# Performance work log

Measured on AMD Instinct MI355X. Metric: run time of the kernel, lower is better.

Reference implementation:

```python
import jax, jax.numpy as jnp
import numpy as np

E = 512      # room_emb_size
H = 8        # nhead
HD = E // H  # head dim
F = 32       # dim_feedforward (hardcoded in source)
L = 3        # num_layers
V = 32000    # voc_size
B = 128      # batch
T = 16       # max_sent_len == max_length
SOS = 1      # sos_idx
EPS = 1e-5   # torch LayerNorm eps


def setup_inputs() -> dict:
    key = jax.random.key(0)
    ks = jax.random.split(key, 10)
    s = 0.02
    def rn(k, shape):
        return jax.random.normal(k, shape, jnp.float32) * s
    return {
        "cur_room_emb": jax.random.normal(ks[0], (B, E), jnp.float32),
        "emb": rn(ks[1], (V, E)),
        "sa_in_w": rn(ks[2], (L, 3 * E, E)), "sa_in_b": jnp.zeros((L, 3 * E), jnp.float32),
        "sa_out_w": rn(ks[3], (L, E, E)), "sa_out_b": jnp.zeros((L, E), jnp.float32),
        "ca_in_w": rn(ks[4], (L, 3 * E, E)), "ca_in_b": jnp.zeros((L, 3 * E), jnp.float32),
        "ca_out_w": rn(ks[5], (L, E, E)), "ca_out_b": jnp.zeros((L, E), jnp.float32),
        "ff1_w": rn(ks[6], (L, F, E)), "ff1_b": jnp.zeros((L, F), jnp.float32),
        "ff2_w": rn(ks[7], (L, E, F)), "ff2_b": jnp.zeros((L, E), jnp.float32),
        "ln_g": jnp.ones((L, 3, E), jnp.float32), "ln_b": jnp.zeros((L, 3, E), jnp.float32),
        "out_w": rn(ks[8], (V, E)), "out_b": jnp.zeros((V,), jnp.float32),
        "max_length": T,
    }


def _ln(x, g, b):
    m = jnp.mean(x, axis=-1, keepdims=True)
    v = jnp.mean((x - m) ** 2, axis=-1, keepdims=True)
    return (x - m) / jnp.sqrt(v + EPS) * g + b


def _mha(qx, kvx, in_w, in_b, out_w, out_b):
    # qx: [Sq,B,E], kvx: [Sk,B,E]  (torch seq-first layout)
    wq, wk, wv = in_w[:E], in_w[E:2 * E], in_w[2 * E:]
    bq, bk, bv = in_b[:E], in_b[E:2 * E], in_b[2 * E:]
    q = (qx @ wq.T + bq).reshape(qx.shape[0], -1, H, HD)
    k = (kvx @ wk.T + bk).reshape(kvx.shape[0], -1, H, HD)
    v = (kvx @ wv.T + bv).reshape(kvx.shape[0], -1, H, HD)
    att = jax.nn.softmax(jnp.einsum('qbhd,kbhd->bhqk', q, k) / np.sqrt(HD).astype(np.float32), axis=-1)
    o = jnp.einsum('bhqk,kbhd->qbhd', att, v).reshape(qx.shape[0], -1, E)
    return o @ out_w.T + out_b


def _pos_enc(n):
    pos = np.arange(n)[:, None].astype(np.float32)
    div = np.exp(np.arange(0, E, 2).astype(np.float32) * (-np.log(10000.0) / E))
    pe = np.zeros((n, E), np.float32)
    pe[:, 0::2] = np.sin(pos * div)
    pe[:, 1::2] = np.cos(pos * div)
    return jnp.asarray(pe)


def reference(cur_room_emb, emb, sa_in_w, sa_in_b, sa_out_w, sa_out_b,
              ca_in_w, ca_in_b, ca_out_w, ca_out_b,
              ff1_w, ff1_b, ff2_w, ff2_b, ln_g, ln_b, out_w, out_b, max_length):
    pe = _pos_enc(max_length)
    bsz = cur_room_emb.shape[0]
    hx = cur_room_emb[None]  # memory [1,B,E]
    # initial <sos> embedding (no positional encoding, as in the source)
    tok_before = jnp.broadcast_to(emb[SOS][None, None, :], (1, bsz, E))
    tokens, probs_all = [], []
    for i in range(max_length):
        x = tok_before  # rerun full decoder over growing history (faithful, no KV cache)
        for l in range(L):
            x = _ln(x + _mha(x, x, sa_in_w[l], sa_in_b[l], sa_out_w[l], sa_out_b[l]), ln_g[l, 0], ln_b[l, 0])
            x = _ln(x + _mha(x, hx, ca_in_w[l], ca_in_b[l], ca_out_w[l], ca_out_b[l]), ln_g[l, 1], ln_b[l, 1])
            ff = jax.nn.relu(x @ ff1_w[l].T + ff1_b[l]) @ ff2_w[l].T + ff2_b[l]
            x = _ln(x + ff, ln_g[l, 2], ln_b[l, 2])
        probs = jax.nn.softmax(x[-1] @ out_w.T + out_b, axis=1)  # emb2idx: Linear + Softmax(dim=1)
        tok = jnp.argmax(probs, axis=1)  # greedy token choice (deterministic)
        tokens.append(tok)
        probs_all.append(probs)
        new = (emb[tok] + pe[i])[None]  # [1,B,E]: embed + positional(i)
        tok_before = jnp.concatenate([tok_before, new], axis=0)
    spoken_token = jnp.stack(tokens, axis=0).T  # [B, max_length]
    return spoken_token, jnp.stack(probs_all, axis=0)  # probs: [T,B,V]
```

## Files before the change

### kernel.cpp

```cpp
#include <hip/hip_runtime.h>
#include <hip/hip_bf16.h>
#include <math.h>

#define E   512
#define E3  1536
#define NH  8
#define FF  32
#define NL  3
#define NV  32000
#define NB  128
#define NT  16
#define RESCUE_DELTA 0.08f

typedef __attribute__((ext_vector_type(8))) short bf16x8;
typedef __attribute__((ext_vector_type(4))) float f32x4;

__global__ void setup_kernel(float* __restrict__ pe, float* __restrict__ tb,
                             const float* __restrict__ emb) {
    const int bi = blockIdx.x;
    if (bi < 16) {
        for (int e = threadIdx.x; e < E; e += blockDim.x) {
            int k = e >> 1;
            double dv = exp((double)(2 * k) * (-log(10000.0) / (double)E));
            double arg = (double)bi * dv;
            pe[bi * E + e] = (e & 1) ? (float)cos(arg) : (float)sin(arg);
        }
    } else {
        const int b = bi - 16;
        for (int e = threadIdx.x; e < E; e += blockDim.x)
            tb[(size_t)b * E + e] = emb[(size_t)1 * E + e];
    }
}

__global__ __launch_bounds__(256) void cvt_bf16_kernel(
    const float* __restrict__ src, unsigned short* __restrict__ dst)
{
    const int i = (blockIdx.x * 256 + threadIdx.x) * 4;
    const float4 v = *(const float4*)&src[i];
    __hip_bfloat16 h0 = __float2bfloat16(v.x);
    __hip_bfloat16 h1 = __float2bfloat16(v.y);
    __hip_bfloat16 h2 = __float2bfloat16(v.z);
    __hip_bfloat16 h3 = __float2bfloat16(v.w);
    dst[i + 0] = *(unsigned short*)&h0;
    dst[i + 1] = *(unsigned short*)&h1;
    dst[i + 2] = *(unsigned short*)&h2;
    dst[i + 3] = *(unsigned short*)&h3;
}

__global__ __launch_bounds__(256) void ca_setup_kernel(
    const float* __restrict__ cur_room,
    const float* __restrict__ ca_in_w, const float* __restrict__ ca_in_b,
    const float* __restrict__ ca_out_w, const float* __restrict__ ca_out_b,
    float* __restrict__ ca_const)
{
    const int b = blockIdx.x, l = blockIdx.y, t = threadIdx.x;
    __shared__ float xl[E];
    __shared__ float hv[E];
    for (int e = t; e < E; e += 256) xl[e] = cur_room[(size_t)b * E + e];
    __syncthreads();
    const float* wv = ca_in_w + ((size_t)l * E3 + 2 * E) * E;
    const float* bv = ca_in_b + (size_t)l * E3 + 2 * E;
    for (int c = t; c < E; c += 256) {
        float s = bv[c];
        const float* wr = wv + (size_t)c * E;
        for (int k = 0; k < E; ++k) s += xl[k] * wr[k];
        hv[c] = s;
    }
    __syncthreads();
    const float* wo = ca_out_w + (size_t)l * E * E;
    for (int c = t; c < E; c += 256) {
        float s = ca_out_b[(size_t)l * E + c];
        const float* wr = wo + (size_t)c * E;
        for (int k = 0; k < E; ++k) s += hv[k] * wr[k];
        ca_const[((size_t)l * NB + b) * E + c] = s;
    }
}

template<bool ADD_BIAS>
__global__ __launch_bounds__(256) void gemm_v3_kernel(
    const float* __restrict__ A, const float* __restrict__ W,
    const float* __restrict__ bias, float* __restrict__ C,
    int N, int K, int KC, size_t CS, int skipm)
{
    const int m0 = blockIdx.y * 64;
    const int n0 = blockIdx.x * 128;
    if (n0 < E && m0 < skipm) return;
    __shared__ float As[16][68];
    __shared__ float Bs[16][132];
    const int tid = threadIdx.x;
    const int kc0 = blockIdx.z * KC;
    const int tx = tid & 15;
    const int ty = tid >> 4;
    const int sr = tid >> 2;
    const int sc = (tid & 3) * 4;

    const float* Ap  = A + (size_t)(m0 + sr) * K + kc0 + sc;
    const float* Wp0 = W + (size_t)(n0 + sr) * K + kc0 + sc;
    const float* Wp1 = W + (size_t)(n0 + 64 + sr) * K + kc0 + sc;

    float4 pa  = *(const float4*)Ap;
    float4 pb0 = *(const float4*)Wp0;
    float4 pb1 = *(const float4*)Wp1;

    float acc[4][8] = {};
    const int nkt = KC >> 4;
    for (int kt = 0; kt < nkt; ++kt) {
        __syncthreads();
        As[sc + 0][sr] = pa.x;  As[sc + 1][sr] = pa.y;
        As[sc + 2][sr] = pa.z;  As[sc + 3][sr] = pa.w;
        Bs[sc + 0][sr] = pb0.x; Bs[sc + 1][sr] = pb0.y;
        Bs[sc + 2][sr] = pb0.z; Bs[sc + 3][sr] = pb0.w;
        Bs[sc + 0][64 + sr] = pb1.x; Bs[sc + 1][64 + sr] = pb1.y;
        Bs[sc + 2][64 + sr] = pb1.z; Bs[sc + 3][64 + sr] = pb1.w;
        __syncthreads();
        if (kt + 1 < nkt) {
            const int off = 16 * (kt + 1);
            pa  = *(const float4*)(Ap + off);
            pb0 = *(const float4*)(Wp0 + off);
            pb1 = *(const float4*)(Wp1 + off);
        }
#pragma unroll
        for (int k = 0; k < 16; ++k) {
            float a[4], b[8];
            *(float4*)&a[0] = *(const float4*)&As[k][ty * 4];
            *(float4*)&b[0] = *(const float4*)&Bs[k][tx * 4];
            *(float4*)&b[4] = *(const float4*)&Bs[k][64 + tx * 4];
#pragma unroll
            for (int i = 0; i < 4; ++i)
#pragma unroll
                for (int j = 0; j < 8; ++j)
                    acc[i][j] += a[i] * b[j];
        }
    }
    float* Co = C + (size_t)blockIdx.z * CS;
#pragma unroll
    for (int i = 0; i < 4; ++i) {
        const int m = m0 + ty * 4 + i;
#pragma unroll
        for (int cj = 0; cj < 2; ++cj) {
            const int n = n0 + cj * 64 + tx * 4;
            float4 o;
            o.x = acc[i][cj * 4 + 0];
            o.y = acc[i][cj * 4 + 1];
            o.z = acc[i][cj * 4 + 2];
            o.w = acc[i][cj * 4 + 3];
            if (ADD_BIAS) {
                const float4 bv = *(const float4*)&bias[n];
                o.x += bv.x; o.y += bv.y; o.z += bv.z; o.w += bv.w;
            }
            *(float4*)&Co[(size_t)m * N + n] = o;
        }
    }
}

__global__ __launch_bounds__(256) void vgemm_bf16_kernel(
    const unsigned short* __restrict__ Abf,
    const unsigned short* __restrict__ Wbf,
    const float* __restrict__ bias, float* __restrict__ Cout)
{
    const int wid = threadIdx.x >> 6, lane = threadIdx.x & 63;
    const int n0 = (blockIdx.x * 4 + wid) * 32;
    const int r = lane & 15;
    const int ko = (lane >> 4) * 8;
    f32x4 acc[2][8];
#pragma unroll
    for (int nt = 0; nt < 2; ++nt)
#pragma unroll
        for (int m = 0; m < 8; ++m)
            acc[nt][m] = (f32x4){0.f, 0.f, 0.f, 0.f};

    const unsigned short* a0 = Abf + (size_t)r * E + ko;
    const unsigned short* w0 = Wbf + (size_t)(n0 + r) * E + ko;
    const unsigned short* w1 = Wbf + (size_t)(n0 + 16 + r) * E + ko;
    for (int k0 = 0; k0 < E; k0 += 32) {
        const bf16x8 b0 = *(const bf16x8*)(w0 + k0);
        const bf16x8 b1 = *(const bf16x8*)(w1 + k0);
#pragma unroll
        for (int m = 0; m < 8; ++m) {
            const bf16x8 af = *(const bf16x8*)(a0 + (size_t)m * 16 * E + k0);
            acc[0][m] = __builtin_amdgcn_mfma_f32_16x16x32_bf16(af, b0, acc[0][m], 0, 0, 0);
            acc[1][m] = __builtin_amdgcn_mfma_f32_16x16x32_bf16(af, b1, acc[1][m], 0, 0, 0);
        }
    }
    const int crow = (lane >> 4) * 4;
#pragma unroll
    for (int nt = 0; nt < 2; ++nt) {
        const int col = n0 + nt * 16 + r;
        const float bv = bias[col];
#pragma unroll
        for (int m = 0; m < 8; ++m)
#pragma unroll
            for (int rr = 0; rr < 4; ++rr)
                Cout[(size_t)(m * 16 + crow + rr) * NV + col] = acc[nt][m][rr] + bv;
    }
}

template<bool WB>
__global__ __launch_bounds__(128) void attn_kernel(
    const float* __restrict__ qkv, size_t QS, int pcount,
    const float* __restrict__ cache, float* __restrict__ wbdst,
    const float* __restrict__ bias,
    float* __restrict__ o, int S, int qstart)
{
    const int b = blockIdx.x >> 3;
    const int h = blockIdx.x & 7;
    __shared__ float Ks[16][64];
    __shared__ float Vs[16][64];
    const int tid = threadIdx.x;
    if (WB) {
        for (int e = tid; e < 192; e += 128) {
            const int part = e >> 6, d = e & 63;
            const int go = part * E + h * 64 + d;
            float v = 0.f;
#pragma unroll
            for (int p = 0; p < 8; ++p) v += qkv[(size_t)p * QS + (size_t)b * E3 + go];
            wbdst[(size_t)b * E3 + go] = v;
            if (part == 1) Ks[S - 1][d] = v + bias[go];
            else if (part == 2) Vs[S - 1][d] = v + bias[go];
        }
        for (int idx = tid; idx < (S - 1) * 64; idx += 128) {
            const int s = idx >> 6, d = idx & 63;
            const size_t base = ((size_t)(s * NB + b)) * E3 + h * 64 + d;
            Ks[s][d] = cache[base + E] + bias[E + h * 64 + d];
            Vs[s][d] = cache[base + 2 * E] + bias[2 * E + h * 64 + d];
        }
    } else {
        for (int idx = tid; idx < S * 64; idx += 128) {
            const int s = idx >> 6, d = idx & 63;
            const size_t base = ((size_t)(s * NB + b)) * E3 + h * 64 + d;
            float kk = bias[E + h * 64 + d];
            float vv = bias[2 * E + h * 64 + d];
            for (int p = 0; p < pcount; ++p) {
                kk += qkv[(size_t)p * QS + base + E];
                vv += qkv[(size_t)p * QS + base + 2 * E];
            }
            Ks[s][d] = kk;
            Vs[s][d] = vv;
        }
    }
    __syncthreads();
    const int wid = tid >> 6, lane = tid & 63;
    const float bq = bias[h * 64 + lane];
    for (int qi = qstart + wid; qi < S; qi += 2) {
        const size_t qbase = ((size_t)(qi * NB + b)) * E3 + h * 64 + lane;
        float qd = bq;
        if (WB) qd += cache[qbase];
        else for (int p = 0; p < pcount; ++p) qd += qkv[(size_t)p * QS + qbase];
        float sc[16];
#pragma unroll
        for (int ki = 0; ki < 16; ++ki) {
            float p = 0.f;
            if (ki < S) {
                p = qd * Ks[ki][lane];
#pragma unroll
                for (int off = 32; off; off >>= 1) p += __shfl_xor(p, off);
                p *= 0.125f;
            }
            sc[ki] = p;
        }
        float m = -1e30f;
#pragma unroll
        for (int ki = 0; ki < 16; ++ki) if (ki < S) m = fmaxf(m, sc[ki]);
        float sum = 0.f;
#pragma unroll
        for (int ki = 0; ki < 16; ++ki) if (ki < S) { sc[ki] = expf(sc[ki] - m); sum += sc[ki]; }
        float inv = 1.0f / sum;
        float acc = 0.f;
#pragma unroll
        for (int ki = 0; ki < 16; ++ki) if (ki < S) acc += sc[ki] * Vs[ki][lane];
        o[((size_t)(qi * NB + b)) * E + h * 64 + lane] = acc * inv;
    }
}

__global__ __launch_bounds__(256) void epilogue_kernel(
    const float* __restrict__ xin,
    const float* __restrict__ yp, size_t YS, int pcount,
    const float* __restrict__ ob,
    const float* __restrict__ ca,
    const float* __restrict__ g0, const float* __restrict__ b0,
    const float* __restrict__ g1, const float* __restrict__ b1,
    const float* __restrict__ w1, const float* __restrict__ b1f,
    const float* __restrict__ w2, const float* __restrict__ b2f,
    const float* __restrict__ g2, const float* __restrict__ bb2,
    float* __restrict__ xout, unsigned short* __restrict__ xbf, int rows)
{
    const int wid = threadIdx.x >> 6, lane = threadIdx.x & 63;
    const int row = blockIdx.x * 4 + wid;
    if (row >= rows) return;
    const float* xr = xin + (size_t)row * E;
    const float* cr = ca + (size_t)(row & (NB - 1)) * E;
    float v[8];
    float s = 0.f;
#pragma unroll
    for (int j = 0; j < 8; ++j) {
        int e = j * 64 + lane;
        float y = xr[e] + ob[e];
        for (int p = 0; p < pcount; ++p) y += yp[(size_t)p * YS + (size_t)row * E + e];
        v[j] = y; s += y;
    }
#pragma unroll
    for (int off = 32; off; off >>= 1) s += __shfl_xor(s, off);
    float mean = s * (1.0f / E);
    float vs = 0.f;
#pragma unroll
    for (int j = 0; j < 8; ++j) { float d = v[j] - mean; vs += d * d; }
#pragma unroll
    for (int off = 32; off; off >>= 1) vs += __shfl_xor(vs, off);
    float rstd = rsqrtf(vs * (1.0f / E) + 1e-5f);
#pragma unroll
    for (int j = 0; j < 8; ++j) {
        int e = j * 64 + lane;
        v[j] = (v[j] - mean) * rstd * g0[e] + b0[e] + cr[e];
    }
    s = 0.f;
#pragma unroll
    for (int j = 0; j < 8; ++j) s += v[j];
#pragma unroll
    for (int off = 32; off; off >>= 1) s += __shfl_xor(s, off);
    mean = s * (1.0f / E);
    vs = 0.f;
#pragma unroll
    for (int j = 0; j < 8; ++j) { float d = v[j] - mean; vs += d * d; }
#pragma unroll
    for (int off = 32; off; off >>= 1) vs += __shfl_xor(vs, off);
    rstd = rsqrtf(vs * (1.0f / E) + 1e-5f);
#pragma unroll
    for (int j = 0; j < 8; ++j) {
        int e = j * 64 + lane;
        v[j] = (v[j] - mean) * rstd * g1[e] + b1[e];
    }
    float h[FF];
#pragma unroll
    for (int f = 0; f < FF; ++f) {
        float p = 0.f;
#pragma unroll
        for (int j = 0; j < 8; ++j) p += v[j] * w1[(size_t)f * E + j * 64 + lane];
#pragma unroll
        for (int off = 32; off; off >>= 1) p += __shfl_xor(p, off);
        h[f] = fmaxf(p + b1f[f], 0.f);
    }
    float o[8];
#pragma unroll
    for (int j = 0; j < 8; ++j) {
        int e = j * 64 + lane;
        float acc = b2f[e];
#pragma unroll
        for (int f4 = 0; f4 < FF / 4; ++f4) {
            float4 w4 = *(const float4*)&w2[(size_t)e * FF + f4 * 4];
            acc += h[f4 * 4 + 0] * w4.x + h[f4 * 4 + 1] * w4.y +
                   h[f4 * 4 + 2] * w4.z + h[f4 * 4 + 3] * w4.w;
        }
        o[j] = v[j] + acc;
    }
    s = 0.f;
#pragma unroll
    for (int j = 0; j < 8; ++j) s += o[j];
#pragma unroll
    for (int off = 32; off; off >>= 1) s += __shfl_xor(s, off);
    mean = s * (1.0f / E);
    vs = 0.f;
#pragma unroll
    for (int j = 0; j < 8; ++j) { float d = o[j] - mean; vs += d * d; }
#pragma unroll
    for (int off = 32; off; off >>= 1) vs += __shfl_xor(vs, off);
    rstd = rsqrtf(vs * (1.0f / E) + 1e-5f);
#pragma unroll
    for (int j = 0; j < 8; ++j) {
        int e = j * 64 + lane;
        const float val = (o[j] - mean) * rstd * g2[e] + bb2[e];
        xout[(size_t)row * E + e] = val;
        if (xbf) {
            __hip_bfloat16 hb = __float2bfloat16(val);
            xbf[(size_t)row * E + e] = *(unsigned short*)&hb;
        }
    }
}

__global__ __launch_bounds__(1024) void softmax_v3_kernel(
    const float* __restrict__ logits,
    const float* __restrict__ xrow,
    const float* __restrict__ out_w,
    const float* __restrict__ ob,
    float* __restrict__ probs_out, float* __restrict__ tok_out,
    const float* __restrict__ emb, const float* __restrict__ pe_row,
    float* __restrict__ tb_new, int step)
{
    const int b = blockIdx.x, t = threadIdx.x;
    const int wid = t >> 6, lane = t & 63;
    const float* L = logits + (size_t)b * NV;
    float r[32];
    float vmax = -1e30f;
#pragma unroll
    for (int j = 0; j < 32; ++j) {
        const int idx = j * 1024 + t;
        if (idx < NV) { r[j] = L[idx]; vmax = fmaxf(vmax, r[j]); }
        else r[j] = -1e30f;
    }
#pragma unroll
    for (int off = 32; off; off >>= 1) vmax = fmaxf(vmax, __shfl_xor(vmax, off));
    __shared__ float swv[16];
    __shared__ float ssum[16];
    __shared__ float sbc[2];
    __shared__ int scnt;
    __shared__ int cand[64];
    __shared__ float cex[64];
    __shared__ int stok;
    if (lane == 0) swv[wid] = vmax;
    if (t == 0) scnt = 0;
    __syncthreads();
    if (t == 0) {
        float m = swv[0];
        for (int w = 1; w < 16; ++w) m = fmaxf(m, swv[w]);
        sbc[0] = m;
    }
    __syncthreads();
    const float m = sbc[0];
#pragma unroll
    for (int j = 0; j < 32; ++j) {
        const int idx = j * 1024 + t;
        if (idx < NV && r[j] >= m - RESCUE_DELTA) {
            const int p = atomicAdd(&scnt, 1);
            if (p < 64) cand[p] = idx;
        }
    }
    __syncthreads();
    const int nc = min(scnt, 64);
    const float* xr = xrow + (size_t)b * E;
    for (int c = wid; c < nc; c += 16) {
        const float* wr = out_w + (size_t)cand[c] * E;
        const float4 a0 = *(const float4*)&xr[lane * 8];
        const float4 a1 = *(const float4*)&xr[lane * 8 + 4];
        const float4 w0 = *(const float4*)&wr[lane * 8];
        const float4 w1 = *(const float4*)&wr[lane * 8 + 4];
        float s = a0.x * w0.x + a0.y * w0.y + a0.z * w0.z + a0.w * w0.w +
                  a1.x * w1.x + a1.y * w1.y + a1.z * w1.z + a1.w * w1.w;
#pragma unroll
        for (int off = 32; off; off >>= 1) s += __shfl_xor(s, off);
        if (lane == 0) cex[c] = s + ob[cand[c]];
    }
    __syncthreads();
    if (t == 0) {
        float bv = -1e30f; int bi = 0x7fffffff;
        for (int c = 0; c < nc; ++c) {
            const float v = cex[c]; const int ii = cand[c];
            if (v > bv || (v == bv && ii < bi)) { bv = v; bi = ii; }
        }
        stok = bi;
    }
    float psum = 0.f;
#pragma unroll
    for (int j = 0; j < 32; ++j) {
        const int idx = j * 1024 + t;
        if (idx < NV) { r[j] = expf(r[j] - m); psum += r[j]; }
    }
#pragma unroll
    for (int off = 32; off; off >>= 1) psum += __shfl_xor(psum, off);
    if (lane == 0) ssum[wid] = psum;
    __syncthreads();
    if (t == 0) {
        float s = 0.f;
        for (int w = 0; w < 16; ++w) s += ssum[w];
        sbc[1] = 1.0f / s;
    }
    __syncthreads();
    const float inv = sbc[1];
    const int tok = stok;
    float* P = probs_out + (size_t)b * NV;
#pragma unroll
    for (int j = 0; j < 32; ++j) {
        const int idx = j * 1024 + t;
        if (idx < NV) P[idx] = r[j] * inv;
    }
    if (t == 0) tok_out[(size_t)b * NT + step] = (float)tok;
    if (t < E) tb_new[(size_t)b * E + t] = emb[(size_t)tok * E + t] + pe_row[t];
}

extern "C" void kernel_launch(void* const* d_in, const int* in_sizes, int n_in,
                              void* d_out, int out_size, void* d_ws, size_t ws_size,
                              hipStream_t stream) {
    const float* cur_room = (const float*)d_in[0];
    const float* emb      = (const float*)d_in[1];
    const float* sa_in_w  = (const float*)d_in[2];
    const float* sa_in_b  = (const float*)d_in[3];
    const float* sa_out_w = (const float*)d_in[4];
    const float* sa_out_b = (const float*)d_in[5];
    const float* ca_in_w  = (const float*)d_in[6];
    const float* ca_in_b  = (const float*)d_in[7];
    const float* ca_out_w = (const float*)d_in[8];
    const float* ca_out_b = (const float*)d_in[9];
    const float* ff1_w    = (const float*)d_in[10];
    const float* ff1_b    = (const float*)d_in[11];
    const float* ff2_w    = (const float*)d_in[12];
    const float* ff2_b    = (const float*)d_in[13];
    const float* ln_g     = (const float*)d_in[14];
    const float* ln_b     = (const float*)d_in[15];
    const float* out_w    = (const float*)d_in[16];
    const float* out_b    = (const float*)d_in[17];
    float* out = (float*)d_out;

    float* ws = (float*)d_ws;
    float* pe       = ws;
    float* ca_const = pe + 16 * E;
    float* tokb     = ca_const + (size_t)NL * NB * E;
    float* x        = tokb + (size_t)17 * NB * E;
    float* qkv0p    = x + (size_t)NT * NB * E;
    float* qkv0     = qkv0p + (size_t)8 * NB * E3;
    float* qkvp     = qkv0 + (size_t)NT * NB * E3;
    float* attn_o   = qkvp + (size_t)32 * NB * E3;
    float* ypart    = attn_o + (size_t)NT * NB * E;
    float* vocp     = ypart + (size_t)4718592;
    unsigned short* wbf = (unsigned short*)(vocp + (size_t)NB * NV);
    unsigned short* xbf = wbf + (size_t)NV * E;

    setup_kernel<<<144, 256, 0, stream>>>(pe, tokb, emb);
    ca_setup_kernel<<<dim3(NB, NL), 256, 0, stream>>>(
        cur_room, ca_in_w, ca_in_b, ca_out_w, ca_out_b, ca_const);
    cvt_bf16_kernel<<<(NV * E) / 1024, 256, 0, stream>>>(out_w, wbf);

    const size_t QS0 = (size_t)NB * E3;

    for (int i = 0; i < NT; ++i) {
        const int S = i + 1;
        const int M = S * NB;
        const size_t QSM = (size_t)M * E3;
        const size_t YSM = (size_t)M * E;

        gemm_v3_kernel<false><<<dim3(E3 / 128, 2, 8), 256, 0, stream>>>(
            tokb + (size_t)i * NB * E, sa_in_w, nullptr, qkv0p, E3, E, 64, QS0, 0);

        const int z_out = (S <= 4) ? 8 : 4;
        for (int l = 0; l < NL; ++l) {
            const float* xin = (l == 0) ? tokb : x;
            const int skipm = (l == 2) ? (S - 1) * NB : 0;
            const int qstart = (l == 2) ? S - 1 : 0;

            if (l == 0) {
                attn_kernel<true><<<NB * NH, 128, 0, stream>>>(
                    qkv0p, QS0, 8, qkv0, qkv0 + (size_t)i * NB * E3,
                    sa_in_b, attn_o, S, 0);
            } else {
                const int z = (S <= 2) ? 8 : (S <= 6) ? 4 : 2;
                gemm_v3_kernel<false><<<dim3(E3 / 128, 2 * S, z), 256, 0, stream>>>(
                    x, sa_in_w + (size_t)l * E3 * E, nullptr, qkvp, E3, E, E / z, QSM, skipm);
                attn_kernel<false><<<NB * NH, 128, 0, stream>>>(
                    qkvp, QSM, z, nullptr, nullptr,
                    sa_in_b + (size_t)l * E3, attn_o, S, qstart);
            }

            if (l == 2) {
                gemm_v3_kernel<false><<<dim3(E / 128, 2, 8), 256, 0, stream>>>(
                    attn_o + (size_t)(S - 1) * NB * E, sa_out_w + (size_t)l * E * E,
                    nullptr, ypart, E, E, 64, (size_t)NB * E, 0);
                epilogue_kernel<<<32, 256, 0, stream>>>(
                    xin + (size_t)(S - 1) * NB * E, ypart, (size_t)NB * E, 8,
                    sa_out_b + (size_t)l * E, ca_const + (size_t)l * NB * E,
                    ln_g + (size_t)(l * 3 + 0) * E, ln_b + (size_t)(l * 3 + 0) * E,
                    ln_g + (size_t)(l * 3 + 1) * E, ln_b + (size_t)(l * 3 + 1) * E,
                    ff1_w + (size_t)l * FF * E, ff1_b + (size_t)l * FF,
                    ff2_w + (size_t)l * E * FF, ff2_b + (size_t)l * E,
                    ln_g + (size_t)(l * 3 + 2) * E, ln_b + (size_t)(l * 3 + 2) * E,
                    x + (size_t)(S - 1) * NB * E, xbf, NB);
            } else {
                gemm_v3_kernel<false><<<dim3(E / 128, 2 * S, z_out), 256, 0, stream>>>(
                    attn_o, sa_out_w + (size_t)l * E * E, nullptr,
                    ypart, E, E, E / z_out, YSM, 0);
                epilogue_kernel<<<S * 32, 256, 0, stream>>>(
                    xin, ypart, YSM, z_out,
                    sa_out_b + (size_t)l * E, ca_const + (size_t)l * NB * E,
                    ln_g + (size_t)(l * 3 + 0) * E, ln_b + (size_t)(l * 3 + 0) * E,
                    ln_g + (size_t)(l * 3 + 1) * E, ln_b + (size_t)(l * 3 + 1) * E,
                    ff1_w + (size_t)l * FF * E, ff1_b + (size_t)l * FF,
                    ff2_w + (size_t)l * E * FF, ff2_b + (size_t)l * E,
                    ln_g + (size_t)(l * 3 + 2) * E, ln_b + (size_t)(l * 3 + 2) * E,
                    x, nullptr, M);
            }
        }
        vgemm_bf16_kernel<<<NV / 128, 256, 0, stream>>>(xbf, wbf, out_b, vocp);
        softmax_v3_kernel<<<NB, 1024, 0, stream>>>(
            vocp, x + (size_t)i * NB * E, out_w, out_b,
            out + 2048 + (size_t)i * NB * NV, out,
            emb, pe + (size_t)i * E, tokb + (size_t)S * NB * E, i);
    }
}
```

Baseline: 4.940 ms.

## Fuse last-layer attention, out-projection, layernorms and FFN into one kernel

For the final decoder layer, replaces the separate attention, out-projection GEMM and epilogue launches with a single per-batch-row kernel. It computes attention for the last query row, a GEMV against the output weight, the three layernorms and the small FFN, and writes the fp32 and bf16 outputs. This removes launches and intermediate buffers per step. In exchange, every block re-reads the full out-projection weight with scalar FP32 math, which may cost more than the launches it removes.

```diff
diff --git a/kernel.cpp b/kernel.cpp
--- a/kernel.cpp
+++ b/kernel.cpp
@@ -282,7 +282,7 @@
     const float* __restrict__ w1, const float* __restrict__ b1f,
     const float* __restrict__ w2, const float* __restrict__ b2f,
     const float* __restrict__ g2, const float* __restrict__ bb2,
-    float* __restrict__ xout, unsigned short* __restrict__ xbf, int rows)
+    float* __restrict__ xout, int rows)
 {
     const int wid = threadIdx.x >> 6, lane = threadIdx.x & 63;
     const int row = blockIdx.x * 4 + wid;
@@ -367,12 +367,172 @@
 #pragma unroll
     for (int j = 0; j < 8; ++j) {
         int e = j * 64 + lane;
-        const float val = (o[j] - mean) * rstd * g2[e] + bb2[e];
-        xout[(size_t)row * E + e] = val;
-        if (xbf) {
-            __hip_bfloat16 hb = __float2bfloat16(val);
-            xbf[(size_t)row * E + e] = *(unsigned short*)&hb;
-        }
+        xout[(size_t)row * E + e] = (o[j] - mean) * rstd * g2[e] + bb2[e];
+    }
+}
+
+__global__ __launch_bounds__(256) void l2_fused_kernel(
+    const float* __restrict__ qkvp, size_t QS, int pcount,
+    const float* __restrict__ bias3,
+    const float* __restrict__ xin,
+    const float* __restrict__ Wout, const float* __restrict__ ob,
+    const float* __restrict__ ca,
+    const float* __restrict__ g0, const float* __restrict__ b0,
+    const float* __restrict__ g1, const float* __restrict__ b1,
+    const float* __restrict__ w1, const float* __restrict__ b1f,
+    const float* __restrict__ w2, const float* __restrict__ b2f,
+    const float* __restrict__ g2, const float* __restrict__ bb2,
+    float* __restrict__ xout, unsigned short* __restrict__ xbf, int S)
+{
+    const int b = blockIdx.x, tid = threadIdx.x;
+    const int w = tid >> 6, lane = tid & 63;
+    __shared__ float ao[E];
+    __shared__ float vsh[E];
+    __shared__ float hsh[FF];
+    __shared__ float sred[4];
+    __shared__ float sbc;
+
+    const size_t qrow = ((size_t)((S - 1) * NB + b)) * E3;
+#pragma unroll
+    for (int hh = 0; hh < 2; ++hh) {
+        const int hd = (w * 2 + hh) * 64 + lane;
+        float q = bias3[hd];
+        for (int p = 0; p < pcount; ++p) q += qkvp[(size_t)p * QS + qrow + hd];
+        float sc[NT];
+        float m = -1e30f;
+        for (int s = 0; s < S; ++s) {
+            const size_t base = ((size_t)(s * NB + b)) * E3 + hd;
+            float kk = bias3[E + hd];
+            for (int p = 0; p < pcount; ++p) kk += qkvp[(size_t)p * QS + base + E];
+            float pd = q * kk;
+#pragma unroll
+            for (int off = 32; off; off >>= 1) pd += __shfl_xor(pd, off);
+            pd *= 0.125f;
+            sc[s] = pd;
+            m = fmaxf(m, pd);
+        }
+        float sum = 0.f;
+        for (int s = 0; s < S; ++s) { sc[s] = expf(sc[s] - m); sum += sc[s]; }
+        const float inv = 1.0f / sum;
+        float acc = 0.f;
+        for (int s = 0; s < S; ++s) {
+            const size_t base = ((size_t)(s * NB + b)) * E3 + hd;
+            float vv = bias3[2 * E + hd];
+            for (int p = 0; p < pcount; ++p) vv += qkvp[(size_t)p * QS + base + 2 * E];
+            acc += sc[s] * vv;
+        }
+        ao[hd] = acc * inv;
+    }
+    __syncthreads();
+
+    float yv[2];
+#pragma unroll
+    for (int half = 0; half < 2; ++half) {
+        const int c = tid + half * 256;
+        const float* wr = Wout + (size_t)c * E;
+        float s = ob[c];
+#pragma unroll 4
+        for (int k = 0; k < E; k += 4) {
+            const float4 a4 = *(const float4*)&ao[k];
+            const float4 w4 = *(const float4*)&wr[k];
+            s += a4.x * w4.x + a4.y * w4.y + a4.z * w4.z + a4.w * w4.w;
+        }
+        yv[half] = s;
+    }
+
+    const float* xr = xin + (size_t)b * E;
+    const float* cr = ca + (size_t)b * E;
+    float v0 = xr[tid] + yv[0];
+    float v1 = xr[tid + 256] + yv[1];
+
+    float s = v0 + v1;
+#pragma unroll
+    for (int off = 32; off; off >>= 1) s += __shfl_xor(s, off);
+    if (lane == 0) sred[w] = s;
+    __syncthreads();
+    float mean = (sred[0] + sred[1] + sred[2] + sred[3]) * (1.0f / E);
+    __syncthreads();
+    float d0 = v0 - mean, d1 = v1 - mean;
+    s = d0 * d0 + d1 * d1;
+#pragma unroll
+    for (int off = 32; off; off >>= 1) s += __shfl_xor(s, off);
+    if (lane == 0) sred[w] = s;
+    __syncthreads();
+    float rstd = rsqrtf((sred[0] + sred[1] + sred[2] + sred[3]) * (1.0f / E) + 1e-5f);
+    __syncthreads();
+    v0 = (v0 - mean) * rstd * g0[tid] + b0[tid] + cr[tid];
+    v1 = (v1 - mean) * rstd * g0[tid + 256] + b0[tid + 256] + cr[tid + 256];
+
+    s = v0 + v1;
+#pragma unroll
+    for (int off = 32; off; off >>= 1) s += __shfl_xor(s, off);
+    if (lane == 0) sred[w] = s;
+    __syncthreads();
+    mean = (sred[0] + sred[1] + sred[2] + sred[3]) * (1.0f / E);
+    __syncthreads();
+    d0 = v0 - mean; d1 = v1 - mean;
+    s = d0 * d0 + d1 * d1;
+#pragma unroll
+    for (int off = 32; off; off >>= 1) s += __shfl_xor(s, off);
+    if (lane == 0) sred[w] = s;
+    __syncthreads();
+    rstd = rsqrtf((sred[0] + sred[1] + sred[2] + sred[3]) * (1.0f / E) + 1e-5f);
+    __syncthreads();
+    v0 = (v0 - mean) * rstd * g1[tid] + b1[tid];
+    v1 = (v1 - mean) * rstd * g1[tid + 256] + b1[tid + 256];
+    vsh[tid] = v0;
+    vsh[tid + 256] = v1;
+    __syncthreads();
+
+    for (int ff = 0; ff < 8; ++ff) {
+        const int f = w * 8 + ff;
+        const float* wr = w1 + (size_t)f * E;
+        float p = 0.f;
+#pragma unroll
+        for (int j = 0; j < 8; ++j) p += vsh[j * 64 + lane] * wr[j * 64 + lane];
+#pragma unroll
+        for (int off = 32; off; off >>= 1) p += __shfl_xor(p, off);
+        if (lane == 0) hsh[f] = fmaxf(p + b1f[f], 0.f);
+    }
+    __syncthreads();
+
+    float o0, o1;
+#pragma unroll
+    for (int half = 0; half < 2; ++half) {
+        const int e = tid + half * 256;
+        float acc = b2f[e];
+#pragma unroll
+        for (int f4 = 0; f4 < FF / 4; ++f4) {
+            const float4 w4 = *(const float4*)&w2[(size_t)e * FF + f4 * 4];
+            acc += hsh[f4 * 4 + 0] * w4.x + hsh[f4 * 4 + 1] * w4.y +
+                   hsh[f4 * 4 + 2] * w4.z + hsh[f4 * 4 + 3] * w4.w;
+        }
+        if (half == 0) o0 = v0 + acc; else o1 = v1 + acc;
+    }
+
+    s = o0 + o1;
+#pragma unroll
+    for (int off = 32; off; off >>= 1) s += __shfl_xor(s, off);
+    if (lane == 0) sred[w] = s;
+    __syncthreads();
+    mean = (sred[0] + sred[1] + sred[2] + sred[3]) * (1.0f / E);
+    __syncthreads();
+    d0 = o0 - mean; d1 = o1 - mean;
+    s = d0 * d0 + d1 * d1;
+#pragma unroll
+    for (int off = 32; off; off >>= 1) s += __shfl_xor(s, off);
+    if (lane == 0) sred[w] = s;
+    __syncthreads();
+    rstd = rsqrtf((sred[0] + sred[1] + sred[2] + sred[3]) * (1.0f / E) + 1e-5f);
+    (void)sbc;
+#pragma unroll
+    for (int half = 0; half < 2; ++half) {
+        const int e = tid + half * 256;
+        const float ov = half ? o1 : o0;
+        const float val = (ov - mean) * rstd * g2[e] + bb2[e];
+        xout[(size_t)b * E + e] = val;
+        __hip_bfloat16 hb = __float2bfloat16(val);
+        xbf[(size_t)b * E + e] = *(unsigned short*)&hb;
     }
 }
 
@@ -529,10 +689,8 @@
             tokb + (size_t)i * NB * E, sa_in_w, nullptr, qkv0p, E3, E, 64, QS0, 0);
 
         const int z_out = (S <= 4) ? 8 : 4;
-        for (int l = 0; l < NL; ++l) {
+        for (int l = 0; l < 2; ++l) {
             const float* xin = (l == 0) ? tokb : x;
-            const int skipm = (l == 2) ? (S - 1) * NB : 0;
-            const int qstart = (l == 2) ? S - 1 : 0;
 
             if (l == 0) {
                 attn_kernel<true><<<NB * NH, 128, 0, stream>>>(
@@ -541,40 +699,44 @@
             } else {
                 const int z = (S <= 2) ? 8 : (S <= 6) ? 4 : 2;
                 gemm_v3_kernel<false><<<dim3(E3 / 128, 2 * S, z), 256, 0, stream>>>(
-                    x, sa_in_w + (size_t)l * E3 * E, nullptr, qkvp, E3, E, E / z, QSM, skipm);
+                    x, sa_in_w + (size_t)l * E3 * E, nullptr, qkvp, E3, E, E / z, QSM, 0);
                 attn_kernel<false><<<NB * NH, 128, 0, stream>>>(
                     qkvp, QSM, z, nullptr, nullptr,
-                    sa_in_b + (size_t)l * E3, attn_o, S, qstart);
+                    sa_in_b + (size_t)l * E3, attn_o, S, 0);
             }
-
-            if (l == 2) {
-                gemm_v3_kernel<false><<<dim3(E / 128, 2, 8), 256, 0, stream>>>(
-                    attn_o + (size_t)(S - 1) * NB * E, sa_out_w + (size_t)l * E * E,
-                    nullptr, ypart, E, E, 64, (size_t)NB * E, 0);
-                epilogue_kernel<<<32, 256, 0, stream>>>(
-                    xin + (size_t)(S - 1) * NB * E, ypart, (size_t)NB * E, 8,
-                    sa_out_b + (size_t)l * E, ca_const + (size_t)l * NB * E,
-                    ln_g + (size_t)(l * 3 + 0) * E, ln_b + (size_t)(l * 3 + 0) * E,
-                    ln_g + (size_t)(l * 3 + 1) * E, ln_b + (size_t)(l * 3 + 1) * E,
-                    ff1_w + (size_t)l * FF * E, ff1_b + (size_t)l * FF,
-                    ff2_w + (size_t)l * E * FF, ff2_b + (size_t)l * E,
-                    ln_g + (size_t)(l * 3 + 2) * E, ln_b + (size_t)(l * 3 + 2) * E,
-                    x + (size_t)(S - 1) * NB * E, xbf, NB);
-            } else {
-                gemm_v3_kernel<false><<<dim3(E / 128, 2 * S, z_out), 256, 0, stream>>>(
-                    attn_o, sa_out_w + (size_t)l * E * E, nullptr,
-                    ypart, E, E, E / z_out, YSM, 0);
-                epilogue_kernel<<<S * 32, 256, 0, stream>>>(
-                    xin, ypart, YSM, z_out,
-                    sa_out_b + (size_t)l * E, ca_const + (size_t)l * NB * E,
-                    ln_g + (size_t)(l * 3 + 0) * E, ln_b + (size_t)(l * 3 + 0) * E,
-                    ln_g + (size_t)(l * 3 + 1) * E, ln_b + (size_t)(l * 3 + 1) * E,
-                    ff1_w + (size_t)l * FF * E, ff1_b + (size_t)l * FF,
-                    ff2_w + (size_t)l * E * FF, ff2_b + (size_t)l * E,
-                    ln_g + (size_t)(l * 3 + 2) * E, ln_b + (size_t)(l * 3 + 2) * E,
-                    x, nullptr, M);
-            }
-        }
+            gemm_v3_kernel<false><<<dim3(E / 128, 2 * S, z_out), 256, 0, stream>>>(
+                attn_o, sa_out_w + (size_t)l * E * E, nullptr,
+                ypart, E, E, E / z_out, YSM, 0);
+            epilogue_kernel<<<S * 32, 256, 0, stream>>>(
+                xin, ypart, YSM, z_out,
+                sa_out_b + (size_t)l * E, ca_const + (size_t)l * NB * E,
+                ln_g + (size_t)(l * 3 + 0) * E, ln_b + (size_t)(l * 3 + 0) * E,
+                ln_g + (size_t)(l * 3 + 1) * E, ln_b + (size_t)(l * 3 + 1) * E,
+                ff1_w + (size_t)l * FF * E, ff1_b + (size_t)l * FF,
+                ff2_w + (size_t)l * E * FF, ff2_b + (size_t)l * E,
+                ln_g + (size_t)(l * 3 + 2) * E, ln_b + (size_t)(l * 3 + 2) * E,
+                x, M);
+        }
+
+        {
+            const int l = 2;
+            const int z = (S <= 2) ? 8 : (S <= 6) ? 4 : 2;
+            gemm_v3_kernel<false><<<dim3(E3 / 128, 2 * S, z), 256, 0, stream>>>(
+                x, sa_in_w + (size_t)l * E3 * E, nullptr, qkvp, E3, E, E / z, QSM,
+                (S - 1) * NB);
+            l2_fused_kernel<<<NB, 256, 0, stream>>>(
+                qkvp, QSM, z, sa_in_b + (size_t)l * E3,
+                x + (size_t)(S - 1) * NB * E,
+                sa_out_w + (size_t)l * E * E, sa_out_b + (size_t)l * E,
+                ca_const + (size_t)l * NB * E,
+                ln_g + (size_t)(l * 3 + 0) * E, ln_b + (size_t)(l * 3 + 0) * E,
+                ln_g + (size_t)(l * 3 + 1) * E, ln_b + (size_t)(l * 3 + 1) * E,
+                ff1_w + (size_t)l * FF * E, ff1_b + (size_t)l * FF,
+                ff2_w + (size_t)l * E * FF, ff2_b + (size_t)l * E,
+                ln_g + (size_t)(l * 3 + 2) * E, ln_b + (size_t)(l * 3 + 2) * E,
+                x + (size_t)(S - 1) * NB * E, xbf, S);
+        }
+
         vgemm_bf16_kernel<<<NV / 128, 256, 0, stream>>>(xbf, wbf, out_b, vocp);
         softmax_v3_kernel<<<NB, 1024, 0, stream>>>(
             vocp, x + (size_t)i * NB * E, out_w, out_b,
```

After: 5.156 ms. 1.04x slower.
